# Kernel tuning notes

Measured on AMD Instinct MI355X. Metric: run time of the kernel, lower is better.

Reference implementation:

```python
import jax, jax.numpy as jnp
import numpy as np

HID = 256
N, D, K, EPOCHS = 100000, 512, 5, 2


def _lin(x, w, b):
    return x @ w.T + b


def setup_inputs() -> dict:
    key = jax.random.key(0)
    ks = jax.random.split(key, 16)
    s = 0.05
    return {
        "x0": jax.random.normal(ks[0], (N, D), jnp.float32),
        "x1": jax.random.normal(ks[1], (N, D), jnp.float32),
        "Hin0_w": jax.random.normal(ks[2], (HID, D), jnp.float32) * s,
        "Hin0_b": jax.random.normal(ks[3], (HID,), jnp.float32) * s,
        "Hin1_w": jax.random.normal(ks[4], (HID, D), jnp.float32) * s,
        "Hin1_b": jax.random.normal(ks[5], (HID,), jnp.float32) * s,
        "w0_w": jax.random.normal(ks[6], (HID, HID), jnp.float32) * s,
        "w0_b": jax.random.normal(ks[7], (HID,), jnp.float32) * s,
        "w1_w": jax.random.normal(ks[8], (HID, HID), jnp.float32) * s,
        "w1_b": jax.random.normal(ks[9], (HID,), jnp.float32) * s,
        "w2_w": jax.random.normal(ks[10], (HID, HID), jnp.float32) * s,
        "w2_b": jax.random.normal(ks[11], (HID,), jnp.float32) * s,
        "edge0": jax.random.randint(ks[12], (2, N * K), 0, N, dtype=jnp.int32),
        "edge1": jax.random.randint(ks[13], (2, N * K), 0, N, dtype=jnp.int32),
        "k": K,
        "update_epoch": EPOCHS,
    }


def reference(x0, x1, Hin0_w, Hin0_b, Hin1_w, Hin1_b, w0_w, w0_b,
              w1_w, w1_b, w2_w, w2_b, edge0, edge1, k, update_epoch):
    xs = (x0, x1)
    edges = (edge0, edge1)
    Hws = ((Hin0_w, Hin0_b), (Hin1_w, Hin1_b))
    n_views = len(xs)

    # per-view input projections: h_init[v] = H_ins[v](train_view[v])
    h_inits = [_lin(x, w, b) for x, (w, b) in zip(xs, Hws)]

    finals = []
    for v in range(n_views):
        # neighbor table: node i's k neighbors are edge[1][i*k : (i+1)*k]
        nbr_idx = edges[v][1].reshape(-1, k)  # [N, k]
        # cross-view self term: mean over other views of w2(h_init_other)
        slf = _lin(h_inits[1 - v], w2_w, w2_b)  # [N, HID] (nv-1 == 1)
        h = h_inits[v]
        for _ in range(update_epoch):
            h = _lin(h, w0_w, w0_b)
            # mean_j w1(h[nbr_j]) == w1(mean_j h[nbr_j]) since w1 is affine
            nbr_mean = h[nbr_idx].mean(axis=1)  # [N, HID] gather + reduce
            h = h + _lin(nbr_mean, w1_w, w1_b) + slf
        finals.append(jax.nn.relu(h))

    # average final embeddings across views
    h_out = sum(finals) / n_views
    return h_out
```

## Files before the change

### kernel.cpp

```cpp
#include <hip/hip_runtime.h>

#define NN 100000
#define DD 512
#define HH 256
#define KNB 5

typedef __attribute__((ext_vector_type(8))) short short8v;
typedef __attribute__((ext_vector_type(4))) short short4v;
typedef __attribute__((ext_vector_type(4))) float float4v;

static __device__ __forceinline__ float bf2f(unsigned short u) {
  union { unsigned int i; float f; } c;
  c.i = ((unsigned int)u) << 16;
  return c.f;
}
static __device__ __forceinline__ unsigned short f2bf(float f) {
  union { float f; unsigned int i; } c;
  c.f = f;
  unsigned int u = c.i;
  u += 0x7FFFu + ((u >> 16) & 1u);
  return (unsigned short)(u >> 16);
}

#define GLOAD16(g, l) __builtin_amdgcn_global_load_lds( \
    (const __attribute__((address_space(1))) unsigned int*)(g), \
    (__attribute__((address_space(3))) unsigned int*)(l), 16, 0, 0)

__global__ void cvt2(const float* __restrict__ s0, short* __restrict__ d0,
                     const float* __restrict__ s1, short* __restrict__ d1) {
  const int S1 = (HH * DD) / 4;
  int i = blockIdx.x * blockDim.x + threadIdx.x;
  if (i >= 2 * S1) return;
  const float* s = (i < S1) ? s0 : s1;
  short* d = (i < S1) ? d0 : d1;
  int j = (i < S1) ? i : i - S1;
  float4 v = reinterpret_cast<const float4*>(s)[j];
  short4v o;
  o[0] = (short)f2bf(v.x); o[1] = (short)f2bf(v.y);
  o[2] = (short)f2bf(v.z); o[3] = (short)f2bf(v.w);
  reinterpret_cast<short4v*>(d)[j] = o;
}

__global__ void prep_w01(const float* __restrict__ w0, const float* __restrict__ w1,
                         const float* __restrict__ w2, const float* __restrict__ b0,
                         const float* __restrict__ b1, const float* __restrict__ b2,
                         short* __restrict__ Bcat, float* __restrict__ bc) {
  int i = blockIdx.x;
  int j = threadIdx.x;
  Bcat[(size_t)i * 768 + j]       = (short)f2bf(w0[i * 256 + j]);
  Bcat[(size_t)i * 768 + 512 + j] = (short)f2bf(w2[i * 256 + j]);
  float acc = 0.f;
  for (int k = 0; k < 256; ++k)
    acc = fmaf(w1[i * 256 + k], w0[k * 256 + j], acc);
  Bcat[(size_t)i * 768 + 256 + j] = (short)f2bf(acc);
  if (j == 0) {
    float s = b0[i] + b1[i] + b2[i];
    for (int k = 0; k < 256; ++k) s = fmaf(w1[i * 256 + k], b0[k], s);
    bc[i] = s;
  }
}

__global__ __launch_bounds__(512, 6) void proj_k(
    const float* __restrict__ Af0, const float* __restrict__ Af1,
    const short* __restrict__ Bw0, const short* __restrict__ Bw1,
    const float* __restrict__ bi0, const float* __restrict__ bi1,
    short* __restrict__ Cb0, short* __restrict__ Cb1)
{
  const float* Af = blockIdx.y ? Af1 : Af0;
  const short* Bw = blockIdx.y ? Bw1 : Bw0;
  const float* bias = blockIdx.y ? bi1 : bi0;
  short* Cb = blockIdx.y ? Cb1 : Cb0;

  __shared__ __align__(16) char BsRaw[256 * 64 * 2];
  __shared__ __align__(16) char AsRaw[64 * 64 * 2];

  const int tid = threadIdx.x;
  const int lane = tid & 63;
  const int wave = tid >> 6;
  const int wr = wave >> 2;
  const int wc = wave & 3;
  const int row0 = blockIdx.x * 64;

  const int sr = tid >> 3;
  const int spc = tid & 7;
  const int slc = spc ^ (sr & 7);
  const int srg = min(row0 + sr, NN - 1);

  float4v acc[2][4];
#pragma unroll
  for (int m = 0; m < 2; ++m)
#pragma unroll
    for (int n = 0; n < 4; ++n) acc[m][n] = (float4v)0.f;

  for (int k0 = 0; k0 < DD; k0 += 64) {
#pragma unroll
    for (int q = 0; q < 4; ++q) {
      int ch = q * 512 + tid;
      int r = ch >> 3, pc = ch & 7;
      int lc = pc ^ (r & 7);
      GLOAD16(Bw + (size_t)r * DD + k0 + lc * 8, BsRaw + (q * 512 + wave * 64) * 16);
    }
    {
      const float* src = Af + (size_t)srg * DD + k0 + slc * 8;
      float4 f0 = *reinterpret_cast<const float4*>(src);
      float4 f1 = *reinterpret_cast<const float4*>(src + 4);
      short8v o;
      o[0] = (short)f2bf(f0.x); o[1] = (short)f2bf(f0.y);
      o[2] = (short)f2bf(f0.z); o[3] = (short)f2bf(f0.w);
      o[4] = (short)f2bf(f1.x); o[5] = (short)f2bf(f1.y);
      o[6] = (short)f2bf(f1.z); o[7] = (short)f2bf(f1.w);
      *reinterpret_cast<short8v*>(AsRaw + tid * 16) = o;
    }
    __syncthreads();

#pragma unroll
    for (int kk = 0; kk < 2; ++kk) {
      const int ckb = kk * 4 + (lane >> 4);
      short8v a[2], b[4];
#pragma unroll
      for (int n = 0; n < 4; ++n) {
        int rb = wc * 64 + n * 16 + (lane & 15);
        b[n] = *reinterpret_cast<const short8v*>(BsRaw + rb * 128 + ((ckb ^ (rb & 7)) << 4));
      }
#pragma unroll
      for (int m = 0; m < 2; ++m) {
        int ra = wr * 32 + m * 16 + (lane & 15);
        a[m] = *reinterpret_cast<const short8v*>(AsRaw + ra * 128 + ((ckb ^ (ra & 7)) << 4));
      }
#pragma unroll
      for (int m = 0; m < 2; ++m)
#pragma unroll
        for (int n = 0; n < 4; ++n)
          acc[m][n] = __builtin_amdgcn_mfma_f32_16x16x32_bf16(b[n], a[m], acc[m][n], 0, 0, 0);
    }
    __syncthreads();
  }

  const int crow = lane & 15;
  const int cg = (lane >> 4) * 4;
#pragma unroll
  for (int m = 0; m < 2; ++m) {
    int rg = row0 + wr * 32 + m * 16 + crow;
    if (rg >= NN) continue;
#pragma unroll
    for (int n = 0; n < 4; ++n) {
      int colb = wc * 64 + n * 16 + cg;
      size_t off = (size_t)rg * HH + colb;
      float4v bi = *reinterpret_cast<const float4v*>(bias + colb);
      short4v o;
#pragma unroll
      for (int i = 0; i < 4; ++i) o[i] = (short)f2bf(acc[m][n][i] + bi[i]);
      *reinterpret_cast<short4v*>(Cb + off) = o;
    }
  }
}

template<int EPI>
__global__ __launch_bounds__(512, 4) void epoch_k(
    const short* __restrict__ D, const short* __restrict__ Cc,
    const short* __restrict__ Bw, const float* __restrict__ bias,
    short* __restrict__ Ob, float* __restrict__ Of,
    const short* __restrict__ Fin, const int* __restrict__ nbr)
{
  __shared__ __align__(16) char BsRaw[256 * 64 * 2];
  __shared__ __align__(16) char AsRaw[128 * 64 * 2];
  __shared__ int nbrL[128][KNB];

  const int tid = threadIdx.x;
  const int lane = tid & 63;
  const int wave = tid >> 6;
  const int wr = wave >> 2;
  const int wc = wave & 3;
  const int row0 = blockIdx.x * 128;

  for (int e = tid; e < 128 * KNB; e += 512) {
    int r = e / KNB;
    int rg = min(row0 + r, NN - 1);
    nbrL[r][e - r * KNB] = nbr[rg * KNB + (e - r * KNB)];
  }

  float4v acc[4][4];
#pragma unroll
  for (int m = 0; m < 4; ++m)
#pragma unroll
    for (int n = 0; n < 4; ++n) acc[m][n] = (float4v)0.f;

  for (int k0 = 0; k0 < 768; k0 += 64) {
#pragma unroll
    for (int q = 0; q < 4; ++q) {
      int ch = q * 512 + tid;
      int r = ch >> 3, pc = ch & 7;
      int lc = pc ^ (r & 7);
      GLOAD16(Bw + (size_t)r * 768 + k0 + lc * 8, BsRaw + (q * 512 + wave * 64) * 16);
    }
    if (k0 < 256 || k0 >= 512) {
      const short* H = (k0 < 256) ? (D + k0) : (Cc + (k0 - 512));
#pragma unroll
      for (int q = 0; q < 2; ++q) {
        int ch = q * 512 + tid;
        int r = ch >> 3, pc = ch & 7;
        int lc = pc ^ (r & 7);
        int rg = min(row0 + r, NN - 1);
        GLOAD16(H + (size_t)rg * HH + lc * 8, AsRaw + (q * 512 + wave * 64) * 16);
      }
    } else {
      const int kb = k0 - 256;
#pragma unroll
      for (int q = 0; q < 2; ++q) {
        int ch = q * 512 + tid;
        int r = ch >> 3, pc = ch & 7;
        int lc = pc ^ (r & 7);
        float a8[8] = {0.f, 0.f, 0.f, 0.f, 0.f, 0.f, 0.f, 0.f};
#pragma unroll
        for (int j = 0; j < KNB; ++j) {
          int id = nbrL[r][j];
          short8v v = *reinterpret_cast<const short8v*>(D + (size_t)id * HH + kb + lc * 8);
#pragma unroll
          for (int x = 0; x < 8; ++x) a8[x] += bf2f((unsigned short)v[x]);
        }
        short8v o;
#pragma unroll
        for (int x = 0; x < 8; ++x) o[x] = (short)f2bf(a8[x] * 0.2f);
        *reinterpret_cast<short8v*>(AsRaw + ch * 16) = o;
      }
    }
    __syncthreads();

#pragma unroll
    for (int kk = 0; kk < 2; ++kk) {
      const int ckb = kk * 4 + (lane >> 4);
      short8v a[4], b[4];
#pragma unroll
      for (int n = 0; n < 4; ++n) {
        int rb = wc * 64 + n * 16 + (lane & 15);
        b[n] = *reinterpret_cast<const short8v*>(BsRaw + rb * 128 + ((ckb ^ (rb & 7)) << 4));
      }
#pragma unroll
      for (int m = 0; m < 4; ++m) {
        int ra = wr * 64 + m * 16 + (lane & 15);
        a[m] = *reinterpret_cast<const short8v*>(AsRaw + ra * 128 + ((ckb ^ (ra & 7)) << 4));
      }
#pragma unroll
      for (int m = 0; m < 4; ++m)
#pragma unroll
        for (int n = 0; n < 4; ++n)
          acc[m][n] = __builtin_amdgcn_mfma_f32_16x16x32_bf16(b[n], a[m], acc[m][n], 0, 0, 0);
    }
    __syncthreads();
  }

  const int crow = lane & 15;
  const int cg = (lane >> 4) * 4;
#pragma unroll
  for (int m = 0; m < 4; ++m) {
    int rg = row0 + wr * 64 + m * 16 + crow;
    if (rg >= NN) continue;
#pragma unroll
    for (int n = 0; n < 4; ++n) {
      int colb = wc * 64 + n * 16 + cg;
      size_t off = (size_t)rg * HH + colb;
      float4v bi = *reinterpret_cast<const float4v*>(bias + colb);
      float v[4];
#pragma unroll
      for (int i = 0; i < 4; ++i) v[i] = acc[m][n][i] + bi[i];
      if constexpr (EPI >= 2) {
#pragma unroll
        for (int i = 0; i < 4; ++i) v[i] = fmaxf(v[i], 0.f);
      }
      if constexpr (EPI <= 2) {
        short4v o;
#pragma unroll
        for (int i = 0; i < 4; ++i) o[i] = (short)f2bf(v[i]);
        *reinterpret_cast<short4v*>(Ob + off) = o;
      } else {
        short4v f4 = *reinterpret_cast<const short4v*>(Fin + off);
        float4v o;
#pragma unroll
        for (int i = 0; i < 4; ++i)
          o[i] = (v[i] + bf2f((unsigned short)f4[i])) * 0.5f;
        *reinterpret_cast<float4v*>(Of + off) = o;
      }
    }
  }
}

extern "C" void kernel_launch(void* const* d_in, const int* in_sizes, int n_in,
                              void* d_out, int out_size, void* d_ws, size_t ws_size,
                              hipStream_t stream) {
  const float* x0  = (const float*)d_in[0];
  const float* x1  = (const float*)d_in[1];
  const float* wh0 = (const float*)d_in[2];
  const float* bh0 = (const float*)d_in[3];
  const float* wh1 = (const float*)d_in[4];
  const float* bh1 = (const float*)d_in[5];
  const float* w0  = (const float*)d_in[6];
  const float* b0  = (const float*)d_in[7];
  const float* w1  = (const float*)d_in[8];
  const float* b1  = (const float*)d_in[9];
  const float* w2  = (const float*)d_in[10];
  const float* b2  = (const float*)d_in[11];
  const int* e0    = (const int*)d_in[12];
  const int* e1    = (const int*)d_in[13];
  const int* nbr0  = e0 + (size_t)NN * KNB;
  const int* nbr1  = e1 + (size_t)NN * KNB;
  float* out       = (float*)d_out;

  char* ws = (char*)d_ws;
  size_t off = 0;
  auto alloc = [&](size_t bytes) -> void* {
    off = (off + 255) & ~(size_t)255;
    void* p = ws + off;
    off += bytes;
    return p;
  };

  short* Wh0  = (short*)alloc((size_t)HH * DD * 2);
  short* Wh1  = (short*)alloc((size_t)HH * DD * 2);
  short* Bcat = (short*)alloc((size_t)HH * 768 * 2);
  float* bc   = (float*)alloc((size_t)HH * 4);
  const size_t NB = (size_t)NN * HH * 2;
  short* hi0 = (short*)alloc(NB);
  short* hi1 = (short*)alloc(NB);
  short* hb0 = (short*)alloc(NB);
  short* hb1 = (short*)alloc(NB);
  short* f0  = (short*)alloc(NB);

  cvt2<<<dim3(256), dim3(256), 0, stream>>>(wh0, Wh0, wh1, Wh1);
  prep_w01<<<dim3(256), dim3(256), 0, stream>>>(w0, w1, w2, b0, b1, b2, Bcat, bc);

  proj_k<<<dim3((NN + 63) / 64, 2), dim3(512), 0, stream>>>(
      x0, x1, Wh0, Wh1, bh0, bh1, hi0, hi1);

  dim3 ge((NN + 127) / 128);

  epoch_k<0><<<ge, dim3(512), 0, stream>>>(hi0, hi1, Bcat, bc, hb0, nullptr, nullptr, nbr0);
  epoch_k<0><<<ge, dim3(512), 0, stream>>>(hi1, hi0, Bcat, bc, hb1, nullptr, nullptr, nbr1);

  epoch_k<2><<<ge, dim3(512), 0, stream>>>(hb0, hi1, Bcat, bc, f0, nullptr, nullptr, nbr0);
  epoch_k<3><<<ge, dim3(512), 0, stream>>>(hb1, hi0, Bcat, bc, nullptr, out, f0, nbr1);

  (void)in_sizes; (void)n_in; (void)out_size; (void)ws_size;
}
```

Measured before the change: 534.8 us.

## Double-buffer LDS tiles in projection GEMM to overlap loads with MFMA

The input projection kernel now keeps two LDS buffers for the weight and activation tiles and prefetches the next K-slice while MFMAs run on the current one, with a single barrier per step. This is meant to hide global load latency behind compute. In exchange LDS use doubles to 80KB per block, so launch bounds drop from 6 to 4 and occupancy falls.

```diff
diff --git a/kernel.cpp b/kernel.cpp
--- a/kernel.cpp
+++ b/kernel.cpp
@@ -60,7 +60,7 @@
   }
 }
 
-__global__ __launch_bounds__(512, 6) void proj_k(
+__global__ __launch_bounds__(512, 4) void proj_k(
     const float* __restrict__ Af0, const float* __restrict__ Af1,
     const short* __restrict__ Bw0, const short* __restrict__ Bw1,
     const float* __restrict__ bi0, const float* __restrict__ bi1,
@@ -71,8 +71,8 @@
   const float* bias = blockIdx.y ? bi1 : bi0;
   short* Cb = blockIdx.y ? Cb1 : Cb0;
 
-  __shared__ __align__(16) char BsRaw[256 * 64 * 2];
-  __shared__ __align__(16) char AsRaw[64 * 64 * 2];
+  __shared__ __align__(16) char BsRaw[2 * 256 * 64 * 2];
+  __shared__ __align__(16) char AsRaw[2 * 64 * 64 * 2];
 
   const int tid = threadIdx.x;
   const int lane = tid & 63;
@@ -82,8 +82,7 @@
   const int row0 = blockIdx.x * 64;
 
   const int sr = tid >> 3;
-  const int spc = tid & 7;
-  const int slc = spc ^ (sr & 7);
+  const int slc = (tid & 7) ^ (sr & 7);
   const int srg = min(row0 + sr, NN - 1);
 
   float4v acc[2][4];
@@ -92,46 +91,72 @@
 #pragma unroll
     for (int n = 0; n < 4; ++n) acc[m][n] = (float4v)0.f;
 
-  for (int k0 = 0; k0 < DD; k0 += 64) {
-#pragma unroll
-    for (int q = 0; q < 4; ++q) {
-      int ch = q * 512 + tid;
-      int r = ch >> 3, pc = ch & 7;
-      int lc = pc ^ (r & 7);
-      GLOAD16(Bw + (size_t)r * DD + k0 + lc * 8, BsRaw + (q * 512 + wave * 64) * 16);
+#pragma unroll
+  for (int q = 0; q < 4; ++q) {
+    int ch = q * 512 + tid;
+    int r = ch >> 3, pc = ch & 7;
+    int lc = pc ^ (r & 7);
+    GLOAD16(Bw + (size_t)r * DD + lc * 8, BsRaw + (q * 512 + wave * 64) * 16);
+  }
+  {
+    const float* src = Af + (size_t)srg * DD + slc * 8;
+    float4 f0 = *reinterpret_cast<const float4*>(src);
+    float4 f1 = *reinterpret_cast<const float4*>(src + 4);
+    short8v o;
+    o[0] = (short)f2bf(f0.x); o[1] = (short)f2bf(f0.y);
+    o[2] = (short)f2bf(f0.z); o[3] = (short)f2bf(f0.w);
+    o[4] = (short)f2bf(f1.x); o[5] = (short)f2bf(f1.y);
+    o[6] = (short)f2bf(f1.z); o[7] = (short)f2bf(f1.w);
+    *reinterpret_cast<short8v*>(AsRaw + tid * 16) = o;
+  }
+  __syncthreads();
+
+  for (int s = 0; s < 8; ++s) {
+    float4 p0, p1;
+    if (s < 7) {
+      char* Bn = BsRaw + ((s + 1) & 1) * 32768;
+#pragma unroll
+      for (int q = 0; q < 4; ++q) {
+        int ch = q * 512 + tid;
+        int r = ch >> 3, pc = ch & 7;
+        int lc = pc ^ (r & 7);
+        GLOAD16(Bw + (size_t)r * DD + (s + 1) * 64 + lc * 8, Bn + (q * 512 + wave * 64) * 16);
+      }
+      const float* src = Af + (size_t)srg * DD + (s + 1) * 64 + slc * 8;
+      p0 = *reinterpret_cast<const float4*>(src);
+      p1 = *reinterpret_cast<const float4*>(src + 4);
     }
     {
-      const float* src = Af + (size_t)srg * DD + k0 + slc * 8;
-      float4 f0 = *reinterpret_cast<const float4*>(src);
-      float4 f1 = *reinterpret_cast<const float4*>(src + 4);
+      const char* Bc = BsRaw + (s & 1) * 32768;
+      const char* Ac = AsRaw + (s & 1) * 8192;
+#pragma unroll
+      for (int kk = 0; kk < 2; ++kk) {
+        const int ckb = kk * 4 + (lane >> 4);
+        short8v a[2], b[4];
+#pragma unroll
+        for (int n = 0; n < 4; ++n) {
+          int rb = wc * 64 + n * 16 + (lane & 15);
+          b[n] = *reinterpret_cast<const short8v*>(Bc + rb * 128 + ((ckb ^ (rb & 7)) << 4));
+        }
+#pragma unroll
+        for (int m = 0; m < 2; ++m) {
+          int ra = wr * 32 + m * 16 + (lane & 15);
+          a[m] = *reinterpret_cast<const short8v*>(Ac + ra * 128 + ((ckb ^ (ra & 7)) << 4));
+        }
+#pragma unroll
+        for (int m = 0; m < 2; ++m)
+#pragma unroll
+          for (int n = 0; n < 4; ++n)
+            acc[m][n] = __builtin_amdgcn_mfma_f32_16x16x32_bf16(b[n], a[m], acc[m][n], 0, 0, 0);
+      }
+    }
+    if (s < 7) {
       short8v o;
-      o[0] = (short)f2bf(f0.x); o[1] = (short)f2bf(f0.y);
-      o[2] = (short)f2bf(f0.z); o[3] = (short)f2bf(f0.w);
-      o[4] = (short)f2bf(f1.x); o[5] = (short)f2bf(f1.y);
-      o[6] = (short)f2bf(f1.z); o[7] = (short)f2bf(f1.w);
-      *reinterpret_cast<short8v*>(AsRaw + tid * 16) = o;
-    }
-    __syncthreads();
-
-#pragma unroll
-    for (int kk = 0; kk < 2; ++kk) {
-      const int ckb = kk * 4 + (lane >> 4);
-      short8v a[2], b[4];
-#pragma unroll
-      for (int n = 0; n < 4; ++n) {
-        int rb = wc * 64 + n * 16 + (lane & 15);
-        b[n] = *reinterpret_cast<const short8v*>(BsRaw + rb * 128 + ((ckb ^ (rb & 7)) << 4));
-      }
-#pragma unroll
-      for (int m = 0; m < 2; ++m) {
-        int ra = wr * 32 + m * 16 + (lane & 15);
-        a[m] = *reinterpret_cast<const short8v*>(AsRaw + ra * 128 + ((ckb ^ (ra & 7)) << 4));
-      }
-#pragma unroll
-      for (int m = 0; m < 2; ++m)
-#pragma unroll
-        for (int n = 0; n < 4; ++n)
-          acc[m][n] = __builtin_amdgcn_mfma_f32_16x16x32_bf16(b[n], a[m], acc[m][n], 0, 0, 0);
+      o[0] = (short)f2bf(p0.x); o[1] = (short)f2bf(p0.y);
+      o[2] = (short)f2bf(p0.z); o[3] = (short)f2bf(p0.w);
+      o[4] = (short)f2bf(p1.x); o[5] = (short)f2bf(p1.y);
+      o[6] = (short)f2bf(p1.z); o[7] = (short)f2bf(p1.w);
+      *reinterpret_cast<short8v*>(AsRaw + ((s + 1) & 1) * 8192 + tid * 16) = o;
     }
     __syncthreads();
   }
```

Measured after the change: 535.0 us. About the same (+0.0%).

## Widen projection blocks to 1024 threads and batch both views' first epoch

Applied to the files above, without the earlier changes.

The projection kernel now runs 1024 threads per block with 16 waves, each computing a 32x32 tile, and each thread loads a single float4 of the activation tile. The first-epoch kernel gains a second grid dimension that selects the view, so both views' epoch-0 work runs in one launch instead of two. The aim is more waves per block to hide memory latency and fewer launch gaps. In exchange each wave has less MFMA work per LDS load, and the larger blocks may limit occupancy.

```diff
diff --git a/kernel.cpp b/kernel.cpp
--- a/kernel.cpp
+++ b/kernel.cpp
@@ -60,7 +60,7 @@
   }
 }
 
-__global__ __launch_bounds__(512, 6) void proj_k(
+__global__ __launch_bounds__(1024, 8) void proj_k(
     const float* __restrict__ Af0, const float* __restrict__ Af1,
     const short* __restrict__ Bw0, const short* __restrict__ Bw1,
     const float* __restrict__ bi0, const float* __restrict__ bi1,
@@ -77,60 +77,58 @@
   const int tid = threadIdx.x;
   const int lane = tid & 63;
   const int wave = tid >> 6;
-  const int wr = wave >> 2;
-  const int wc = wave & 3;
+  const int wrr = wave >> 3;
+  const int wcc = wave & 7;
   const int row0 = blockIdx.x * 64;
 
-  const int sr = tid >> 3;
-  const int spc = tid & 7;
-  const int slc = spc ^ (sr & 7);
+  const int sr = tid >> 4;
+  const int slc = ((tid >> 1) & 7) ^ (sr & 7);
+  const int shf = tid & 1;
   const int srg = min(row0 + sr, NN - 1);
-
-  float4v acc[2][4];
+  const float* Asrc = Af + (size_t)srg * DD + slc * 8 + shf * 4;
+  const int sdst = (tid >> 1) * 16 + shf * 8;
+
+  float4v acc[2][2];
 #pragma unroll
   for (int m = 0; m < 2; ++m)
 #pragma unroll
-    for (int n = 0; n < 4; ++n) acc[m][n] = (float4v)0.f;
+    for (int n = 0; n < 2; ++n) acc[m][n] = (float4v)0.f;
 
   for (int k0 = 0; k0 < DD; k0 += 64) {
 #pragma unroll
-    for (int q = 0; q < 4; ++q) {
-      int ch = q * 512 + tid;
+    for (int q = 0; q < 2; ++q) {
+      int ch = q * 1024 + tid;
       int r = ch >> 3, pc = ch & 7;
       int lc = pc ^ (r & 7);
-      GLOAD16(Bw + (size_t)r * DD + k0 + lc * 8, BsRaw + (q * 512 + wave * 64) * 16);
+      GLOAD16(Bw + (size_t)r * DD + k0 + lc * 8, BsRaw + (q * 1024 + wave * 64) * 16);
     }
     {
-      const float* src = Af + (size_t)srg * DD + k0 + slc * 8;
-      float4 f0 = *reinterpret_cast<const float4*>(src);
-      float4 f1 = *reinterpret_cast<const float4*>(src + 4);
-      short8v o;
-      o[0] = (short)f2bf(f0.x); o[1] = (short)f2bf(f0.y);
-      o[2] = (short)f2bf(f0.z); o[3] = (short)f2bf(f0.w);
-      o[4] = (short)f2bf(f1.x); o[5] = (short)f2bf(f1.y);
-      o[6] = (short)f2bf(f1.z); o[7] = (short)f2bf(f1.w);
-      *reinterpret_cast<short8v*>(AsRaw + tid * 16) = o;
+      float4 f = *reinterpret_cast<const float4*>(Asrc + k0);
+      short4v o;
+      o[0] = (short)f2bf(f.x); o[1] = (short)f2bf(f.y);
+      o[2] = (short)f2bf(f.z); o[3] = (short)f2bf(f.w);
+      *reinterpret_cast<short4v*>(AsRaw + sdst) = o;
     }
     __syncthreads();
 
 #pragma unroll
     for (int kk = 0; kk < 2; ++kk) {
       const int ckb = kk * 4 + (lane >> 4);
-      short8v a[2], b[4];
-#pragma unroll
-      for (int n = 0; n < 4; ++n) {
-        int rb = wc * 64 + n * 16 + (lane & 15);
+      short8v a[2], b[2];
+#pragma unroll
+      for (int n = 0; n < 2; ++n) {
+        int rb = wcc * 32 + n * 16 + (lane & 15);
         b[n] = *reinterpret_cast<const short8v*>(BsRaw + rb * 128 + ((ckb ^ (rb & 7)) << 4));
       }
 #pragma unroll
       for (int m = 0; m < 2; ++m) {
-        int ra = wr * 32 + m * 16 + (lane & 15);
+        int ra = wrr * 32 + m * 16 + (lane & 15);
         a[m] = *reinterpret_cast<const short8v*>(AsRaw + ra * 128 + ((ckb ^ (ra & 7)) << 4));
       }
 #pragma unroll
       for (int m = 0; m < 2; ++m)
 #pragma unroll
-        for (int n = 0; n < 4; ++n)
+        for (int n = 0; n < 2; ++n)
           acc[m][n] = __builtin_amdgcn_mfma_f32_16x16x32_bf16(b[n], a[m], acc[m][n], 0, 0, 0);
     }
     __syncthreads();
@@ -140,11 +138,11 @@
   const int cg = (lane >> 4) * 4;
 #pragma unroll
   for (int m = 0; m < 2; ++m) {
-    int rg = row0 + wr * 32 + m * 16 + crow;
+    int rg = row0 + wrr * 32 + m * 16 + crow;
     if (rg >= NN) continue;
 #pragma unroll
-    for (int n = 0; n < 4; ++n) {
-      int colb = wc * 64 + n * 16 + cg;
+    for (int n = 0; n < 2; ++n) {
+      int colb = wcc * 32 + n * 16 + cg;
       size_t off = (size_t)rg * HH + colb;
       float4v bi = *reinterpret_cast<const float4v*>(bias + colb);
       short4v o;
@@ -157,14 +155,21 @@
 
 template<int EPI>
 __global__ __launch_bounds__(512, 4) void epoch_k(
-    const short* __restrict__ D, const short* __restrict__ Cc,
+    const short* __restrict__ D0_, const short* __restrict__ C0_,
+    short* __restrict__ O0_, const int* __restrict__ n0_,
+    const short* __restrict__ D1_, const short* __restrict__ C1_,
+    short* __restrict__ O1_, const int* __restrict__ n1_,
     const short* __restrict__ Bw, const float* __restrict__ bias,
-    short* __restrict__ Ob, float* __restrict__ Of,
-    const short* __restrict__ Fin, const int* __restrict__ nbr)
+    float* __restrict__ Of, const short* __restrict__ Fin)
 {
   __shared__ __align__(16) char BsRaw[256 * 64 * 2];
   __shared__ __align__(16) char AsRaw[128 * 64 * 2];
   __shared__ int nbrL[128][KNB];
+
+  const short* D  = blockIdx.y ? D1_ : D0_;
+  const short* Cc = blockIdx.y ? C1_ : C0_;
+  short* Ob       = blockIdx.y ? O1_ : O0_;
+  const int* nbr  = blockIdx.y ? n1_ : n0_;
 
   const int tid = threadIdx.x;
   const int lane = tid & 63;
@@ -328,16 +333,19 @@
   cvt2<<<dim3(256), dim3(256), 0, stream>>>(wh0, Wh0, wh1, Wh1);
   prep_w01<<<dim3(256), dim3(256), 0, stream>>>(w0, w1, w2, b0, b1, b2, Bcat, bc);
 
-  proj_k<<<dim3((NN + 63) / 64, 2), dim3(512), 0, stream>>>(
+  proj_k<<<dim3((NN + 63) / 64, 2), dim3(1024), 0, stream>>>(
       x0, x1, Wh0, Wh1, bh0, bh1, hi0, hi1);
 
   dim3 ge((NN + 127) / 128);
 
-  epoch_k<0><<<ge, dim3(512), 0, stream>>>(hi0, hi1, Bcat, bc, hb0, nullptr, nullptr, nbr0);
-  epoch_k<0><<<ge, dim3(512), 0, stream>>>(hi1, hi0, Bcat, bc, hb1, nullptr, nullptr, nbr1);
-
-  epoch_k<2><<<ge, dim3(512), 0, stream>>>(hb0, hi1, Bcat, bc, f0, nullptr, nullptr, nbr0);
-  epoch_k<3><<<ge, dim3(512), 0, stream>>>(hb1, hi0, Bcat, bc, nullptr, out, f0, nbr1);
+  epoch_k<0><<<dim3(ge.x, 2), dim3(512), 0, stream>>>(
+      hi0, hi1, hb0, nbr0,  hi1, hi0, hb1, nbr1,  Bcat, bc, nullptr, nullptr);
+
+  epoch_k<2><<<dim3(ge.x, 1), dim3(512), 0, stream>>>(
+      hb0, hi1, f0, nbr0,   hb0, hi1, f0, nbr0,   Bcat, bc, nullptr, nullptr);
+
+  epoch_k<3><<<dim3(ge.x, 1), dim3(512), 0, stream>>>(
+      hb1, hi0, nullptr, nbr1,  hb1, hi0, nullptr, nbr1,  Bcat, bc, out, f0);
 
   (void)in_sizes; (void)n_in; (void)out_size; (void)ws_size;
 }
```

After: 527.4 us. No clear change (-1.4%).

## Stage full x tile in LDS, stream weights from registers, merge view launches

Applied to the files above, without the earlier changes.

The projection kernel now converts the whole 64x512 input tile to bf16 in LDS once, with a single barrier, instead of looping over K-chunks. Weight fragments are read straight from global memory into registers with one-step prefetch, which removes the per-chunk LDS staging of B and the paired barriers. The first-epoch kernels for both views are merged into one launch using blockIdx.y, cutting launch count and tail effects. The cost is 64KB of LDS per block (occupancy hint lowered to 4) and weight reads that depend on L2 hits, with no reuse through LDS.

```diff
diff --git a/kernel.cpp b/kernel.cpp
--- a/kernel.cpp
+++ b/kernel.cpp
@@ -60,7 +60,7 @@
   }
 }
 
-__global__ __launch_bounds__(512, 6) void proj_k(
+__global__ __launch_bounds__(512, 4) void proj_k(
     const float* __restrict__ Af0, const float* __restrict__ Af1,
     const short* __restrict__ Bw0, const short* __restrict__ Bw1,
     const float* __restrict__ bi0, const float* __restrict__ bi1,
@@ -71,8 +71,7 @@
   const float* bias = blockIdx.y ? bi1 : bi0;
   short* Cb = blockIdx.y ? Cb1 : Cb0;
 
-  __shared__ __align__(16) char BsRaw[256 * 64 * 2];
-  __shared__ __align__(16) char AsRaw[64 * 64 * 2];
+  __shared__ __align__(16) char AsRaw[64 * 512 * 2];
 
   const int tid = threadIdx.x;
   const int lane = tid & 63;
@@ -81,59 +80,66 @@
   const int wc = wave & 3;
   const int row0 = blockIdx.x * 64;
 
-  const int sr = tid >> 3;
-  const int spc = tid & 7;
-  const int slc = spc ^ (sr & 7);
-  const int srg = min(row0 + sr, NN - 1);
-
-  float4v acc[2][4];
-#pragma unroll
-  for (int m = 0; m < 2; ++m)
-#pragma unroll
-    for (int n = 0; n < 4; ++n) acc[m][n] = (float4v)0.f;
-
-  for (int k0 = 0; k0 < DD; k0 += 64) {
-#pragma unroll
-    for (int q = 0; q < 4; ++q) {
-      int ch = q * 512 + tid;
-      int r = ch >> 3, pc = ch & 7;
-      int lc = pc ^ (r & 7);
-      GLOAD16(Bw + (size_t)r * DD + k0 + lc * 8, BsRaw + (q * 512 + wave * 64) * 16);
-    }
-    {
-      const float* src = Af + (size_t)srg * DD + k0 + slc * 8;
-      float4 f0 = *reinterpret_cast<const float4*>(src);
-      float4 f1 = *reinterpret_cast<const float4*>(src + 4);
+  {
+    const int r = tid >> 3;
+    const int rg = min(row0 + r, NN - 1);
+    const float* xrow = Af + (size_t)rg * DD;
+#pragma unroll
+    for (int q = 0; q < 8; ++q) {
+      int lc = (tid & 7) + q * 8;
+      const float* s = xrow + lc * 8;
+      float4 f0 = *reinterpret_cast<const float4*>(s);
+      float4 f1 = *reinterpret_cast<const float4*>(s + 4);
       short8v o;
       o[0] = (short)f2bf(f0.x); o[1] = (short)f2bf(f0.y);
       o[2] = (short)f2bf(f0.z); o[3] = (short)f2bf(f0.w);
       o[4] = (short)f2bf(f1.x); o[5] = (short)f2bf(f1.y);
       o[6] = (short)f2bf(f1.z); o[7] = (short)f2bf(f1.w);
-      *reinterpret_cast<short8v*>(AsRaw + tid * 16) = o;
-    }
-    __syncthreads();
-
-#pragma unroll
-    for (int kk = 0; kk < 2; ++kk) {
-      const int ckb = kk * 4 + (lane >> 4);
-      short8v a[2], b[4];
-#pragma unroll
-      for (int n = 0; n < 4; ++n) {
-        int rb = wc * 64 + n * 16 + (lane & 15);
-        b[n] = *reinterpret_cast<const short8v*>(BsRaw + rb * 128 + ((ckb ^ (rb & 7)) << 4));
-      }
-#pragma unroll
-      for (int m = 0; m < 2; ++m) {
-        int ra = wr * 32 + m * 16 + (lane & 15);
-        a[m] = *reinterpret_cast<const short8v*>(AsRaw + ra * 128 + ((ckb ^ (ra & 7)) << 4));
-      }
-#pragma unroll
-      for (int m = 0; m < 2; ++m)
-#pragma unroll
-        for (int n = 0; n < 4; ++n)
-          acc[m][n] = __builtin_amdgcn_mfma_f32_16x16x32_bf16(b[n], a[m], acc[m][n], 0, 0, 0);
-    }
-    __syncthreads();
+      *reinterpret_cast<short8v*>(AsRaw + r * 1024 + ((lc ^ (r & 7)) << 4)) = o;
+    }
+  }
+  __syncthreads();
+
+  float4v acc[2][4];
+#pragma unroll
+  for (int m = 0; m < 2; ++m)
+#pragma unroll
+    for (int n = 0; n < 4; ++n) acc[m][n] = (float4v)0.f;
+
+  const int rbl = lane & 15;
+  const int kh = (lane >> 4) * 8;
+  const short* Bbase[4];
+#pragma unroll
+  for (int n = 0; n < 4; ++n)
+    Bbase[n] = Bw + (size_t)(wc * 64 + n * 16 + rbl) * DD + kh;
+
+  short8v pb[4];
+#pragma unroll
+  for (int n = 0; n < 4; ++n)
+    pb[n] = *reinterpret_cast<const short8v*>(Bbase[n]);
+
+#pragma unroll
+  for (int kk = 0; kk < 16; ++kk) {
+    short8v b[4];
+#pragma unroll
+    for (int n = 0; n < 4; ++n) b[n] = pb[n];
+    if (kk < 15) {
+#pragma unroll
+      for (int n = 0; n < 4; ++n)
+        pb[n] = *reinterpret_cast<const short8v*>(Bbase[n] + (kk + 1) * 32);
+    }
+    const int lca = kk * 4 + (lane >> 4);
+    short8v a[2];
+#pragma unroll
+    for (int m = 0; m < 2; ++m) {
+      int ra = wr * 32 + m * 16 + (lane & 15);
+      a[m] = *reinterpret_cast<const short8v*>(AsRaw + ra * 1024 + ((lca ^ (ra & 7)) << 4));
+    }
+#pragma unroll
+    for (int m = 0; m < 2; ++m)
+#pragma unroll
+      for (int n = 0; n < 4; ++n)
+        acc[m][n] = __builtin_amdgcn_mfma_f32_16x16x32_bf16(b[n], a[m], acc[m][n], 0, 0, 0);
   }
 
   const int crow = lane & 15;
@@ -157,14 +163,21 @@
 
 template<int EPI>
 __global__ __launch_bounds__(512, 4) void epoch_k(
-    const short* __restrict__ D, const short* __restrict__ Cc,
+    const short* __restrict__ D0_, const short* __restrict__ C0_,
+    short* __restrict__ O0_, const int* __restrict__ n0_,
+    const short* __restrict__ D1_, const short* __restrict__ C1_,
+    short* __restrict__ O1_, const int* __restrict__ n1_,
     const short* __restrict__ Bw, const float* __restrict__ bias,
-    short* __restrict__ Ob, float* __restrict__ Of,
-    const short* __restrict__ Fin, const int* __restrict__ nbr)
+    float* __restrict__ Of, const short* __restrict__ Fin)
 {
   __shared__ __align__(16) char BsRaw[256 * 64 * 2];
   __shared__ __align__(16) char AsRaw[128 * 64 * 2];
   __shared__ int nbrL[128][KNB];
+
+  const short* D  = blockIdx.y ? D1_ : D0_;
+  const short* Cc = blockIdx.y ? C1_ : C0_;
+  short* Ob       = blockIdx.y ? O1_ : O0_;
+  const int* nbr  = blockIdx.y ? n1_ : n0_;
 
   const int tid = threadIdx.x;
   const int lane = tid & 63;
@@ -333,11 +346,14 @@
 
   dim3 ge((NN + 127) / 128);
 
-  epoch_k<0><<<ge, dim3(512), 0, stream>>>(hi0, hi1, Bcat, bc, hb0, nullptr, nullptr, nbr0);
-  epoch_k<0><<<ge, dim3(512), 0, stream>>>(hi1, hi0, Bcat, bc, hb1, nullptr, nullptr, nbr1);
-
-  epoch_k<2><<<ge, dim3(512), 0, stream>>>(hb0, hi1, Bcat, bc, f0, nullptr, nullptr, nbr0);
-  epoch_k<3><<<ge, dim3(512), 0, stream>>>(hb1, hi0, Bcat, bc, nullptr, out, f0, nbr1);
+  epoch_k<0><<<dim3(ge.x, 2), dim3(512), 0, stream>>>(
+      hi0, hi1, hb0, nbr0,  hi1, hi0, hb1, nbr1,  Bcat, bc, nullptr, nullptr);
+
+  epoch_k<2><<<dim3(ge.x, 1), dim3(512), 0, stream>>>(
+      hb0, hi1, f0, nbr0,   hb0, hi1, f0, nbr0,   Bcat, bc, nullptr, nullptr);
+
+  epoch_k<3><<<dim3(ge.x, 1), dim3(512), 0, stream>>>(
+      hb1, hi0, nullptr, nbr1,  hb1, hi0, nullptr, nbr1,  Bcat, bc, out, f0);
 
   (void)in_sizes; (void)n_in; (void)out_size; (void)ws_size;
 }
```

Measured after the change: 636.3 us. 1.19x slower.
